# Optimization experiments

Measured on AMD Instinct MI355X. Metric: run time of the kernel, lower is better.

The kernel has to match this reference:

```python
import jax, jax.numpy as jnp
import numpy as np

DIM, H, DH, MLP, ADIM = 512, 8, 64, 2048, 256
B, T = 4, 2048
EPS = 1e-5


def setup_inputs() -> dict:
    key = jax.random.key(0)
    ks = jax.random.split(key, 10)
    s = 0.02
    inner = H * DH
    return {
        "x": jax.random.normal(ks[0], (B, T, DIM), jnp.float32),
        "action_emb": jax.random.normal(ks[1], (B, T, ADIM), jnp.float32),
        "causal_mask": jnp.tril(jnp.ones((T, T), dtype=bool)),
        "Wqkv": jax.random.normal(ks[2], (3 * inner, DIM), jnp.float32) * s,
        "Wout": jax.random.normal(ks[3], (DIM, inner), jnp.float32) * s,
        "bout": jnp.zeros((DIM,), jnp.float32),
        "W1": jax.random.normal(ks[4], (MLP, DIM), jnp.float32) * s,
        "b1": jnp.zeros((MLP,), jnp.float32),
        "W2": jax.random.normal(ks[5], (DIM, MLP), jnp.float32) * s,
        "b2": jnp.zeros((DIM,), jnp.float32),
        # adaLN is zero-init in the module; use small random so modulation is exercised
        "Wmod": jax.random.normal(ks[6], (6 * DIM, ADIM), jnp.float32) * s,
        "bmod": jnp.zeros((6 * DIM,), jnp.float32),
    }


def _layernorm(z):
    mu = jnp.mean(z, axis=-1, keepdims=True)
    var = jnp.var(z, axis=-1, keepdims=True)
    return (z - mu) * jax.lax.rsqrt(var + EPS)


def reference(x, action_emb, causal_mask, Wqkv, Wout, bout, W1, b1, W2, b2, Wmod, bmod):
    b, t, d = x.shape
    mod = jax.nn.silu(action_emb) @ Wmod.T + bmod            # (B,T,6*dim)
    shift1, scale1, gate1, shift2, scale2, gate2 = jnp.split(mod, 6, axis=-1)

    h = _layernorm(x) * (1.0 + scale1) + shift1
    qkv = (h @ Wqkv.T).reshape(b, t, 3, H, DH)
    q, k, v = qkv[:, :, 0], qkv[:, :, 1], qkv[:, :, 2]        # (B,T,H,DH)
    scores = jnp.einsum("bqhd,bkhd->bhqk", q, k) * (DH ** -0.5)
    scores = jnp.where(causal_mask, scores, -jnp.inf)
    attn = jax.nn.softmax(scores, axis=-1)                   # dropout=eval (identity)
    h = jnp.einsum("bhqk,bkhd->bqhd", attn, v).reshape(b, t, H * DH)
    h = h @ Wout.T + bout
    x = x + gate1 * h

    h = _layernorm(x) * (1.0 + scale2) + shift2
    h = jax.nn.gelu(h @ W1.T + b1, approximate=False) @ W2.T + b2
    return x + gate2 * h
```

## Files before the change

kernel.cpp:

```cpp
#include <hip/hip_runtime.h>
#include <math.h>
#include <stdint.h>

#define BB 4
#define TT 2048
#define NTOK 8192
#define DIMD 512
#define HH 8
#define DHH 64
#define MLPD 2048
#define ADIMD 256
#define MODD 3072
#define LNEPS 1e-5f
#define LOG2E_8 0.18033688011112042f
#define PBLK 4224

typedef short short8 __attribute__((ext_vector_type(8)));
typedef unsigned short ushort4v __attribute__((ext_vector_type(4)));
typedef __bf16 bf16x8 __attribute__((ext_vector_type(8)));
typedef float f32x4 __attribute__((ext_vector_type(4)));

static __device__ __forceinline__ unsigned short f2bf(float f) {
    return __builtin_bit_cast(unsigned short, (__bf16)f);
}
static __device__ __forceinline__ float bf2f(unsigned short u) {
    union { unsigned u; float f; } v; v.u = (unsigned)u << 16; return v.f;
}
static __device__ __forceinline__ unsigned pk2bf(float a, float b) {
    return (unsigned)f2bf(a) | ((unsigned)f2bf(b) << 16);
}

static __device__ __forceinline__ f32x4 mfma_bf16(short8 a, short8 b, f32x4 c) {
    return __builtin_amdgcn_mfma_f32_16x16x32_bf16(
        __builtin_bit_cast(bf16x8, a), __builtin_bit_cast(bf16x8, b), c, 0, 0, 0);
}

static __device__ __forceinline__ void gload_lds16(const void* g, void* l) {
    __builtin_amdgcn_global_load_lds(
        (const __attribute__((address_space(1))) unsigned int*)g,
        (__attribute__((address_space(3))) unsigned int*)l, 16, 0, 0);
}

struct CvtArgs {
    const float* s[6];
    unsigned short* d[6];
    int cum[7];
};
__global__ __launch_bounds__(256) void cvt_all(CvtArgs a)
{
    const int i = blockIdx.x * 256 + threadIdx.x;
    if (i >= a.cum[6]) return;
    int seg = 0;
    #pragma unroll
    for (int k = 1; k < 6; k++) seg += (i >= a.cum[k]);
    const int off = i - a.cum[seg];
    float4 v = ((const float4*)a.s[seg])[off];
    if (seg == 5) {
        v.x = v.x / (1.f + __expf(-v.x));
        v.y = v.y / (1.f + __expf(-v.y));
        v.z = v.z / (1.f + __expf(-v.z));
        v.w = v.w / (1.f + __expf(-v.w));
    }
    uint2 o;
    o.x = pk2bf(v.x, v.y);
    o.y = pk2bf(v.z, v.w);
    ((uint2*)a.d[seg])[off] = o;
}

template<int EPI, int BN>
__global__ __launch_bounds__(256, (BN == 128 ? 4 : 6)) void gemm_bf16(
    const unsigned short* __restrict__ A, const unsigned short* __restrict__ Bw,
    const float* __restrict__ bias, const float* __restrict__ res,
    const unsigned short* __restrict__ mod,
    int M, int N, int K,
    void* __restrict__ Cv)
{
    constexpr int MT = (BN == 128) ? 4 : 2;
    constexpr int NPB = (BN == 128) ? 4 : 2;
    __shared__ unsigned short As[128 * 64];
    __shared__ unsigned short Bs[BN * 64];

    const int tid = threadIdx.x;
    const int w = tid >> 6, lane = tid & 63;
    const int quad = lane >> 4, l16 = lane & 15;
    const int wrow = (BN == 128) ? (w >> 1) * 64 : w * 32;
    const int wcol = (BN == 128) ? (w & 1) * 64 : 0;
    const int row0 = blockIdx.y * 128, col0 = blockIdx.x * BN;

    const int srow = tid >> 3;
    const int skc  = (tid & 7) * 8;

    f32x4 acc[MT][4];
    #pragma unroll
    for (int i = 0; i < MT; i++)
        #pragma unroll
        for (int j = 0; j < 4; j++) acc[i][j] = (f32x4){0.f, 0.f, 0.f, 0.f};

    auto stage_async = [&](int k0) {
        #pragma unroll
        for (int p = 0; p < 4; p++)
            gload_lds16(&A[(size_t)(row0 + srow + p * 32) * K + k0 + skc],
                        &As[p * 2048 + tid * 8]);
        #pragma unroll
        for (int p = 0; p < NPB; p++)
            gload_lds16(&Bw[(size_t)(col0 + srow + p * 32) * K + k0 + skc],
                        &Bs[p * 2048 + tid * 8]);
    };

    stage_async(0);
    __syncthreads();

    for (int k0 = 0; k0 < K; k0 += 64) {
        #pragma unroll
        for (int ks = 0; ks < 2; ks++) {
            short8 af[MT], bf[4];
            #pragma unroll
            for (int mt = 0; mt < MT; mt++)
                af[mt] = *(const short8*)&As[(wrow + mt * 16 + l16) * 64 + ks * 32 + quad * 8];
            #pragma unroll
            for (int nt = 0; nt < 4; nt++)
                bf[nt] = *(const short8*)&Bs[(wcol + nt * 16 + l16) * 64 + ks * 32 + quad * 8];
            #pragma unroll
            for (int nt = 0; nt < 4; nt++)
                #pragma unroll
                for (int mt = 0; mt < MT; mt++)
                    acc[mt][nt] = mfma_bf16(af[mt], bf[nt], acc[mt][nt]);
        }
        __syncthreads();
        if (k0 + 64 < K) stage_async(k0 + 64);
        __syncthreads();
    }

    float* Cf = (float*)Cv;
    unsigned short* Cb = (unsigned short*)Cv;
    #pragma unroll
    for (int mt = 0; mt < MT; mt++) {
        #pragma unroll
        for (int r = 0; r < 4; r++) {
            const int row = row0 + wrow + mt * 16 + quad * 4 + r;
            #pragma unroll
            for (int nt = 0; nt < 4; nt++) {
                const int col = col0 + wcol + nt * 16 + l16;
                const size_t idx = (size_t)row * N + col;
                const float v = acc[mt][nt][r];
                if (EPI == 0) {
                    Cb[idx] = f2bf(v);
                } else if (EPI == 2) {
                    float t = v + bias[col];
                    Cb[idx] = f2bf(0.5f * t * (1.f + erff(t * 0.70710678118654752f)));
                } else if (EPI == 3) {
                    float t = v + bias[col];
                    Cf[idx] = res[idx] + bf2f(mod[(size_t)row * MODD + 1024 + col]) * t;
                } else if (EPI == 4) {
                    float t = v + bias[col];
                    Cf[idx] = Cf[idx] + bf2f(mod[(size_t)row * MODD + 2560 + col]) * t;
                } else if (EPI == 5) {
                    Cb[idx] = f2bf(v + bias[col]);
                }
            }
        }
    }
}

__global__ __launch_bounds__(256) void adaln_ln(
    const float* __restrict__ src, const unsigned short* __restrict__ mod,
    unsigned short* __restrict__ dst, int shift_off, int scale_off)
{
    const int n = blockIdx.x;
    const int tid = threadIdx.x;
    const float* xr = src + (size_t)n * DIMD;
    float v0 = xr[tid], v1 = xr[tid + 256];
    float s = v0 + v1;
    float q = v0 * v0 + v1 * v1;
    #pragma unroll
    for (int o = 32; o > 0; o >>= 1) {
        s += __shfl_down(s, o);
        q += __shfl_down(q, o);
    }
    __shared__ float sh[8];
    __shared__ float mu_sh, rs_sh;
    const int wid = tid >> 6, lane = tid & 63;
    if (lane == 0) { sh[wid] = s; sh[wid + 4] = q; }
    __syncthreads();
    if (tid == 0) {
        float S = sh[0] + sh[1] + sh[2] + sh[3];
        float Q = sh[4] + sh[5] + sh[6] + sh[7];
        float mu = S * (1.f / DIMD);
        float var = Q * (1.f / DIMD) - mu * mu;
        mu_sh = mu;
        rs_sh = rsqrtf(var + LNEPS);
    }
    __syncthreads();
    const float mu = mu_sh, rs = rs_sh;
    const unsigned short* mrow = mod + (size_t)n * MODD;
    const size_t o0 = (size_t)n * DIMD + tid;
    dst[o0]       = f2bf((v0 - mu) * rs * (1.f + bf2f(mrow[scale_off + tid]))       + bf2f(mrow[shift_off + tid]));
    dst[o0 + 256] = f2bf((v1 - mu) * rs * (1.f + bf2f(mrow[scale_off + tid + 256])) + bf2f(mrow[shift_off + tid + 256]));
}

__global__ __launch_bounds__(256, 5) void attn_mfma(
    const unsigned short* __restrict__ qkv, float* __restrict__ part)
{
    __shared__ unsigned short Kt[64][76];
    __shared__ unsigned short Vt[64][76];
    __shared__ unsigned short Ps[4][16][76];

    const int f = 79 - (int)blockIdx.x;
    int qi, ch;
    if (f < 8)       { qi = f;               ch = 0; }
    else if (f < 24) { const int g = f - 8;  qi = 8 + (g >> 1);  ch = g & 1; }
    else if (f < 48) { const int g = f - 24; qi = 16 + g / 3;    ch = g % 3; }
    else             { const int g = f - 48; qi = 24 + (g >> 2); ch = g & 3; }

    const int h = blockIdx.y, b = blockIdx.z;
    const int tid = threadIdx.x;
    const int w = tid >> 6;
    const int lane = tid & 63;
    const int quad = lane >> 4;
    const int l16 = lane & 15;

    const int qw = qi * 64 + w * 16;
    const size_t tokbase = (size_t)b * TT;

    short8 qf[2];
    {
        const unsigned short* qp = qkv + (tokbase + qw + l16) * 1536 + h * 64 + quad * 8;
        #pragma unroll
        for (int hd = 0; hd < 2; hd++) {
            short8 raw = *(const short8*)(qp + hd * 32);
            short8 fr;
            #pragma unroll
            for (int j = 0; j < 8; j++)
                fr[j] = (short)f2bf(bf2f((unsigned short)raw[j]) * LOG2E_8);
            qf[hd] = fr;
        }
    }

    f32x4 Oa[4];
    float mrun = -INFINITY, lrun = 0.f;
    #pragma unroll
    for (int mt = 0; mt < 4; mt++) Oa[mt] = (f32x4){0.f, 0.f, 0.f, 0.f};

    const int k0t = ch * 8;
    const int k1t = min(k0t + 8, qi + 1);
    const int vk0 = (tid & 31) * 2;
    const int vdb = (tid >> 5) * 8;

    short8 kpre[2], vpre[2];
    auto prefetchKV = [&](int kt) {
        const unsigned short* kb = qkv + (tokbase + (size_t)kt * 64) * 1536 + 512 + h * 64;
        #pragma unroll
        for (int it = 0; it < 2; it++) {
            const int i = tid + it * 256;
            kpre[it] = *(const short8*)(kb + (size_t)(i >> 3) * 1536 + (i & 7) * 8);
        }
        const unsigned short* vb = qkv + (tokbase + (size_t)kt * 64 + vk0) * 1536 + 1024 + h * 64 + vdb;
        vpre[0] = *(const short8*)vb;
        vpre[1] = *(const short8*)(vb + 1536);
    };
    auto storeKV = [&]() {
        #pragma unroll
        for (int it = 0; it < 2; it++) {
            const int i = tid + it * 256;
            *(short8*)&Kt[i >> 3][(i & 7) * 8] = kpre[it];
        }
        #pragma unroll
        for (int j = 0; j < 8; j++) {
            *(unsigned*)&Vt[vdb + j][vk0] =
                (unsigned)(unsigned short)vpre[0][j]
                | ((unsigned)(unsigned short)vpre[1][j] << 16);
        }
    };

    prefetchKV(k0t);
    storeKV();
    __syncthreads();

    for (int kt = k0t; kt < k1t; kt++) {
        const bool haveNext = (kt + 1 < k1t);
        if (haveNext) prefetchKV(kt + 1);

        f32x4 st[4];
        #pragma unroll
        for (int mk = 0; mk < 4; mk++) {
            const short8 a0 = *(const short8*)&Kt[mk * 16 + l16][quad * 8];
            const short8 a1 = *(const short8*)&Kt[mk * 16 + l16][32 + quad * 8];
            st[mk] = (f32x4){0.f, 0.f, 0.f, 0.f};
            st[mk] = mfma_bf16(a0, qf[0], st[mk]);
            st[mk] = mfma_bf16(a1, qf[1], st[mk]);
        }
        if (kt == qi) {
            const int qrel = w * 16 + l16;
            #pragma unroll
            for (int mk = 0; mk < 4; mk++)
                #pragma unroll
                for (int r = 0; r < 4; r++)
                    if (mk * 16 + quad * 4 + r > qrel) st[mk][r] = -INFINITY;
        }
        float tm = -INFINITY;
        #pragma unroll
        for (int mk = 0; mk < 4; mk++)
            #pragma unroll
            for (int r = 0; r < 4; r++) tm = fmaxf(tm, st[mk][r]);
        tm = fmaxf(tm, __shfl_xor(tm, 16));
        tm = fmaxf(tm, __shfl_xor(tm, 32));
        if (!__all(tm <= mrun + 8.0f)) {
            const float mn = fmaxf(mrun, tm);
            const float alpha = __builtin_amdgcn_exp2f(mrun - mn);
            lrun *= alpha;
            #pragma unroll
            for (int mt = 0; mt < 4; mt++) Oa[mt] *= alpha;
            mrun = mn;
        }
        float ts = 0.f;
        #pragma unroll
        for (int mk = 0; mk < 4; mk++) {
            const float p0 = __builtin_amdgcn_exp2f(st[mk][0] - mrun);
            const float p1 = __builtin_amdgcn_exp2f(st[mk][1] - mrun);
            const float p2 = __builtin_amdgcn_exp2f(st[mk][2] - mrun);
            const float p3 = __builtin_amdgcn_exp2f(st[mk][3] - mrun);
            ts += (p0 + p1) + (p2 + p3);
            const unsigned long long pk =
                (unsigned long long)pk2bf(p0, p1)
                | ((unsigned long long)pk2bf(p2, p3) << 32);
            *(unsigned long long*)&Ps[w][l16][mk * 16 + quad * 4] = pk;
        }
        ts += __shfl_xor(ts, 16);
        ts += __shfl_xor(ts, 32);
        lrun += ts;
        __threadfence_block();

        short8 pf[2];
        #pragma unroll
        for (int kc = 0; kc < 2; kc++)
            pf[kc] = *(const short8*)&Ps[w][l16][kc * 32 + quad * 8];
        #pragma unroll
        for (int mt = 0; mt < 4; mt++)
            #pragma unroll
            for (int kc = 0; kc < 2; kc++) {
                const short8 vf = *(const short8*)&Vt[mt * 16 + l16][kc * 32 + quad * 8];
                Oa[mt] = mfma_bf16(vf, pf[kc], Oa[mt]);
            }

        __syncthreads();
        if (haveNext) storeKV();
        __syncthreads();
    }

    float* pO = part + ((size_t)((b * HH + h) * 80 + f)) * PBLK;
    #pragma unroll
    for (int mt = 0; mt < 4; mt++)
        *(f32x4*)&pO[(w * 16 + l16) * 64 + mt * 16 + quad * 4] = Oa[mt];
    if (quad == 0) {
        pO[4096 + (w * 16 + l16) * 2]     = mrun;
        pO[4096 + (w * 16 + l16) * 2 + 1] = lrun;
    }
}

__global__ __launch_bounds__(256) void attn_combine(
    const float* __restrict__ part, unsigned short* __restrict__ outb)
{
    const int idx = blockIdx.x * 256 + threadIdx.x;
    const int d4 = idx & 15;
    const int h = (idx >> 4) & 7;
    const int tok = idx >> 7;
    const int t = tok & (TT - 1);
    const int b = tok >> 11;
    const int qi = t >> 6;
    const int nch = (qi >> 3) + 1;
    int cum;
    if (qi < 8)       cum = qi;
    else if (qi < 16) cum = 8 + ((qi - 8) << 1);
    else if (qi < 24) cum = 24 + (qi - 16) * 3;
    else              cum = 48 + ((qi - 24) << 2);
    const int qloc = t & 63;
    const float* base = part + ((size_t)((b * HH + h) * 80 + cum)) * PBLK;

    float M = -INFINITY;
    for (int c = 0; c < nch; c++)
        M = fmaxf(M, base[c * PBLK + 4096 + qloc * 2]);
    float L = 0.f, a0 = 0.f, a1 = 0.f, a2 = 0.f, a3 = 0.f;
    for (int c = 0; c < nch; c++) {
        const float m = base[c * PBLK + 4096 + qloc * 2];
        const float l = base[c * PBLK + 4097 + qloc * 2];
        const float sc = __builtin_amdgcn_exp2f(m - M);
        L += l * sc;
        const float4 o = *(const float4*)&base[c * PBLK + qloc * 64 + d4 * 4];
        a0 += sc * o.x; a1 += sc * o.y; a2 += sc * o.z; a3 += sc * o.w;
    }
    const float inv = 1.f / L;
    const unsigned long long pk =
        (unsigned long long)pk2bf(a0 * inv, a1 * inv)
        | ((unsigned long long)pk2bf(a2 * inv, a3 * inv) << 32);
    *(unsigned long long*)&outb[(size_t)tok * DIMD + h * 64 + d4 * 4] = pk;
}

extern "C" void kernel_launch(void* const* d_in, const int* in_sizes, int n_in,
                              void* d_out, int out_size, void* d_ws, size_t ws_size,
                              hipStream_t stream)
{
    (void)in_sizes; (void)n_in; (void)out_size; (void)ws_size;

    const float* x    = (const float*)d_in[0];
    const float* aemb = (const float*)d_in[1];
    const float* Wqkv = (const float*)d_in[3];
    const float* Wout = (const float*)d_in[4];
    const float* bout = (const float*)d_in[5];
    const float* W1   = (const float*)d_in[6];
    const float* b1   = (const float*)d_in[7];
    const float* W2   = (const float*)d_in[8];
    const float* b2   = (const float*)d_in[9];
    const float* Wmod = (const float*)d_in[10];
    const float* bmod = (const float*)d_in[11];

    float* out = (float*)d_out;

    char* p = (char*)d_ws;
    unsigned short* modw = (unsigned short*)p; p += (size_t)NTOK * MODD * 2;
    unsigned short* h12  = (unsigned short*)p; p += (size_t)NTOK * DIMD * 2;
    unsigned short* qkvb = (unsigned short*)p; p += (size_t)NTOK * 1536 * 2;
    unsigned short* attw = (unsigned short*)p; p += (size_t)NTOK * DIMD * 2;
    unsigned short* hid  = qkvb;
    unsigned short* sact = (unsigned short*)p; p += (size_t)NTOK * ADIMD * 2;
    unsigned short* wq = (unsigned short*)p;   p += (size_t)1536 * 512 * 2;
    unsigned short* wo = (unsigned short*)p;   p += (size_t)512 * 512 * 2;
    unsigned short* w1 = (unsigned short*)p;   p += (size_t)2048 * 512 * 2;
    unsigned short* w2 = (unsigned short*)p;   p += (size_t)512 * 2048 * 2;
    unsigned short* wm = (unsigned short*)p;   p += (size_t)3072 * 256 * 2;
    p = (char*)(((uintptr_t)p + 255) & ~(uintptr_t)255);
    float* part = (float*)p;

    CvtArgs ca;
    ca.s[0] = Wqkv; ca.d[0] = wq;
    ca.s[1] = Wout; ca.d[1] = wo;
    ca.s[2] = W1;   ca.d[2] = w1;
    ca.s[3] = W2;   ca.d[3] = w2;
    ca.s[4] = Wmod; ca.d[4] = wm;
    ca.s[5] = aemb; ca.d[5] = sact;
    const int n4s[6] = {1536 * 512 / 4, 512 * 512 / 4, 2048 * 512 / 4,
                        512 * 2048 / 4, 3072 * 256 / 4, NTOK * ADIMD / 4};
    ca.cum[0] = 0;
    for (int i = 0; i < 6; i++) ca.cum[i + 1] = ca.cum[i] + n4s[i];
    cvt_all<<<(ca.cum[6] + 255) / 256, 256, 0, stream>>>(ca);

    gemm_bf16<5, 128><<<dim3(MODD / 128, NTOK / 128), 256, 0, stream>>>(
        sact, wm, bmod, nullptr, nullptr, NTOK, MODD, ADIMD, modw);

    adaln_ln<<<NTOK, 256, 0, stream>>>(x, modw, h12, 0, 512);

    gemm_bf16<0, 128><<<dim3(1536 / 128, NTOK / 128), 256, 0, stream>>>(
        h12, wq, nullptr, nullptr, nullptr, NTOK, 1536, DIMD, qkvb);

    attn_mfma<<<dim3(80, HH, BB), 256, 0, stream>>>(qkvb, part);
    attn_combine<<<NTOK * HH * 16 / 256, 256, 0, stream>>>(part, attw);

    gemm_bf16<3, 64><<<dim3(DIMD / 64, NTOK / 128), 256, 0, stream>>>(
        attw, wo, bout, x, modw, NTOK, DIMD, DIMD, out);

    adaln_ln<<<NTOK, 256, 0, stream>>>(out, modw, h12, 1536, 2048);

    gemm_bf16<2, 128><<<dim3(MLPD / 128, NTOK / 128), 256, 0, stream>>>(
        h12, w1, b1, nullptr, nullptr, NTOK, MLPD, DIMD, hid);

    gemm_bf16<4, 64><<<dim3(DIMD / 64, NTOK / 128), 256, 0, stream>>>(
        hid, w2, b2, nullptr, modw, NTOK, DIMD, MLPD, out);
}
```

Measured before the change: 321.6 us.

## Double-buffer GEMM shared-memory tiles to overlap global loads with MFMA

Splits the GEMM A/B shared-memory tiles into two buffers so the next K-tile is loaded asynchronously while MFMAs run on the current one, leaving one barrier per iteration instead of two. This aims to hide global-to-LDS latency behind compute. It doubles LDS use per block and lowers the launch-bounds occupancy hint (4→2 and 6→3 blocks), so fewer waves may be resident to hide latency.

```diff
diff --git a/kernel.cpp b/kernel.cpp
--- a/kernel.cpp
+++ b/kernel.cpp
@@ -68,7 +68,7 @@
 }
 
 template<int EPI, int BN>
-__global__ __launch_bounds__(256, (BN == 128 ? 4 : 6)) void gemm_bf16(
+__global__ __launch_bounds__(256, (BN == 128 ? 2 : 3)) void gemm_bf16(
     const unsigned short* __restrict__ A, const unsigned short* __restrict__ Bw,
     const float* __restrict__ bias, const float* __restrict__ res,
     const unsigned short* __restrict__ mod,
@@ -76,9 +76,9 @@
     void* __restrict__ Cv)
 {
     constexpr int MT = (BN == 128) ? 4 : 2;
-    constexpr int NPB = (BN == 128) ? 4 : 2;
-    __shared__ unsigned short As[128 * 64];
-    __shared__ unsigned short Bs[BN * 64];
+    constexpr int NPB = BN / 32;
+    __shared__ unsigned short As[2][128 * 64];
+    __shared__ unsigned short Bs[2][BN * 64];
 
     const int tid = threadIdx.x;
     const int w = tid >> 6, lane = tid & 63;
@@ -96,38 +96,40 @@
         #pragma unroll
         for (int j = 0; j < 4; j++) acc[i][j] = (f32x4){0.f, 0.f, 0.f, 0.f};
 
-    auto stage_async = [&](int k0) {
+    auto stage_async = [&](int k0, int buf) {
         #pragma unroll
         for (int p = 0; p < 4; p++)
             gload_lds16(&A[(size_t)(row0 + srow + p * 32) * K + k0 + skc],
-                        &As[p * 2048 + tid * 8]);
+                        &As[buf][p * 2048 + tid * 8]);
         #pragma unroll
         for (int p = 0; p < NPB; p++)
             gload_lds16(&Bw[(size_t)(col0 + srow + p * 32) * K + k0 + skc],
-                        &Bs[p * 2048 + tid * 8]);
+                        &Bs[buf][p * 2048 + tid * 8]);
     };
 
-    stage_async(0);
+    stage_async(0, 0);
     __syncthreads();
 
-    for (int k0 = 0; k0 < K; k0 += 64) {
+    const int nt = K >> 6;
+    for (int t = 0; t < nt; t++) {
+        const int cur = t & 1;
+        if (t + 1 < nt) stage_async((t + 1) << 6, cur ^ 1);
+
         #pragma unroll
         for (int ks = 0; ks < 2; ks++) {
             short8 af[MT], bf[4];
             #pragma unroll
             for (int mt = 0; mt < MT; mt++)
-                af[mt] = *(const short8*)&As[(wrow + mt * 16 + l16) * 64 + ks * 32 + quad * 8];
-            #pragma unroll
-            for (int nt = 0; nt < 4; nt++)
-                bf[nt] = *(const short8*)&Bs[(wcol + nt * 16 + l16) * 64 + ks * 32 + quad * 8];
-            #pragma unroll
-            for (int nt = 0; nt < 4; nt++)
+                af[mt] = *(const short8*)&As[cur][(wrow + mt * 16 + l16) * 64 + ks * 32 + quad * 8];
+            #pragma unroll
+            for (int nt2 = 0; nt2 < 4; nt2++)
+                bf[nt2] = *(const short8*)&Bs[cur][(wcol + nt2 * 16 + l16) * 64 + ks * 32 + quad * 8];
+            #pragma unroll
+            for (int nt2 = 0; nt2 < 4; nt2++)
                 #pragma unroll
                 for (int mt = 0; mt < MT; mt++)
-                    acc[mt][nt] = mfma_bf16(af[mt], bf[nt], acc[mt][nt]);
-        }
-        __syncthreads();
-        if (k0 + 64 < K) stage_async(k0 + 64);
+                    acc[mt][nt2] = mfma_bf16(af[mt], bf[nt2], acc[mt][nt2]);
+        }
         __syncthreads();
     }
 
@@ -139,21 +141,21 @@
         for (int r = 0; r < 4; r++) {
             const int row = row0 + wrow + mt * 16 + quad * 4 + r;
             #pragma unroll
-            for (int nt = 0; nt < 4; nt++) {
-                const int col = col0 + wcol + nt * 16 + l16;
+            for (int nt2 = 0; nt2 < 4; nt2++) {
+                const int col = col0 + wcol + nt2 * 16 + l16;
                 const size_t idx = (size_t)row * N + col;
-                const float v = acc[mt][nt][r];
+                const float v = acc[mt][nt2][r];
                 if (EPI == 0) {
                     Cb[idx] = f2bf(v);
                 } else if (EPI == 2) {
-                    float t = v + bias[col];
-                    Cb[idx] = f2bf(0.5f * t * (1.f + erff(t * 0.70710678118654752f)));
+                    float t2 = v + bias[col];
+                    Cb[idx] = f2bf(0.5f * t2 * (1.f + erff(t2 * 0.70710678118654752f)));
                 } else if (EPI == 3) {
-                    float t = v + bias[col];
-                    Cf[idx] = res[idx] + bf2f(mod[(size_t)row * MODD + 1024 + col]) * t;
+                    float t2 = v + bias[col];
+                    Cf[idx] = res[idx] + bf2f(mod[(size_t)row * MODD + 1024 + col]) * t2;
                 } else if (EPI == 4) {
-                    float t = v + bias[col];
-                    Cf[idx] = Cf[idx] + bf2f(mod[(size_t)row * MODD + 2560 + col]) * t;
+                    float t2 = v + bias[col];
+                    Cf[idx] = Cf[idx] + bf2f(mod[(size_t)row * MODD + 2560 + col]) * t2;
                 } else if (EPI == 5) {
                     Cb[idx] = f2bf(v + bias[col]);
                 }
```

Result: slower. 342.7 us (+6.6%).
